# Performance work log

Measured on AMD Instinct MI355X. Metric: run time of the kernel, lower is better.

The kernel has to match this reference:

```python
import jax, jax.numpy as jnp
import numpy as np

N_NODES = 100000
LATENT_DIM = 8
SAMPLE_SIZE = 8192
N_EDGES = 1000000
EPS = 1e-6


def setup_inputs() -> dict:
    key = jax.random.key(0)
    k1, k2, k3, k4, k5 = jax.random.split(key, 5)
    latent_Z = jax.random.normal(k1, (N_NODES, LATENT_DIM), dtype=jnp.float32)
    alpha = jax.random.normal(k2, (1,), dtype=jnp.float32)
    sample_idx = jax.random.randint(k3, (SAMPLE_SIZE,), 0, N_NODES, dtype=jnp.int64)
    sparse_sample_i = jax.random.randint(k4, (N_EDGES,), 0, N_NODES, dtype=jnp.int64)
    sparse_sample_j = jax.random.randint(k5, (N_EDGES,), 0, N_NODES, dtype=jnp.int64)
    return {"latent_Z": latent_Z, "alpha": alpha, "sample_idx": sample_idx,
            "sparse_sample_i": sparse_sample_i, "sparse_sample_j": sparse_sample_j}


def reference(latent_Z, alpha, sample_idx, sparse_sample_i, sparse_sample_j):
    # --- dense non-edge term over the sampled subgraph ---
    Zs = latent_Z[sample_idx]                              # [S, D]
    diff = Zs[:, None, :] - Zs[None, :, :] + EPS           # [S, S, D]
    dist = jnp.sqrt(jnp.sum(diff * diff, axis=-1))         # [S, S]
    mat = jnp.exp(-dist)                                   # [S, S]
    # original uses exp(ones) vectors in the matmul-with-ones trick -> factor e^2
    ones_exp_sq = jnp.exp(jnp.float32(1.0)) ** 2
    offdiag_sum = jnp.sum(mat) - jnp.sum(jnp.diagonal(mat))
    z_pdist1 = jnp.exp(alpha[0]) * 0.5 * ones_exp_sq * offdiag_sum
    # --- sparse positive-edge term ---
    ed = latent_Z[sparse_sample_i] - latent_Z[sparse_sample_j] + EPS  # [E, D]
    edist = jnp.sqrt(jnp.sum(ed * ed, axis=-1))                        # [E]
    z_pdist2 = jnp.sum(-edist + alpha[0])
    return z_pdist2 - z_pdist1
```

## Files before the change

kernel.cpp:

```cpp
#include <hip/hip_runtime.h>
#include <hip/hip_bf16.h>
#include <math.h>

#define NNODES   100000
#define S        8192
#define D        8
#define EPSF     1e-6f
#define LOG2E    1.442695040888963f
#define EPS_S    (LOG2E * EPSF)
#define NT2      256

#define ZBS_OFF  0
#define U_OFF    131104
#define V_OFF    163872
#define ZB_OFF   196640
#define BK_OFF   1796736

#define NDBLK    2048
#define NWPP     64
#define ZROW     8192

typedef __attribute__((ext_vector_type(8)))  short short8_t;
typedef __attribute__((ext_vector_type(16))) float f32x16;

__device__ __forceinline__ void block_reduce_2(float a, float b, float* sma,
                                               float* smb, float& ra, float& rb) {
    #pragma unroll
    for (int off = 32; off > 0; off >>= 1) {
        a += __shfl_down(a, off, 64);
        b += __shfl_down(b, off, 64);
    }
    int lane = threadIdx.x & 63, wid = threadIdx.x >> 6;
    if (lane == 0) { sma[wid] = a; smb[wid] = b; }
    __syncthreads();
    if (threadIdx.x == 0) {
        ra = 0.f; rb = 0.f;
        for (int w = 0; w < 4; ++w) { ra += sma[w]; rb += smb[w]; }
    }
}

__global__ __launch_bounds__(256) void gather_kernel(const float* __restrict__ Z,
                                                     const int* __restrict__ idx,
                                                     ushort* __restrict__ zbs,
                                                     float* __restrict__ u,
                                                     float* __restrict__ v,
                                                     ushort* __restrict__ zb16,
                                                     char* __restrict__ buckets) {
    int gid = blockIdx.x * 256 + threadIdx.x;

    if (gid < 385) {
        *(double*)(buckets + (size_t)gid * 128) = 0.0;
    }
    if (blockIdx.x == 2 && threadIdx.x == 0) {
        short8_t zz = { 0,0,0,0,0,0,0,0 };
        *(short8_t*)(zbs + (size_t)ZROW * 8) = zz;
    }

    if (gid < S) {
        int n = idx[gid];
        const float4* zp = (const float4*)(Z + (size_t)n * D);
        float4 a = zp[0], b = zp[1];
        float z[8] = { a.x, a.y, a.z, a.w, b.x, b.y, b.z, b.w };
        float ss = 0.f;
        short8_t h;
        #pragma unroll
        for (int k = 0; k < 8; ++k) {
            float zs = LOG2E * z[k];
            __hip_bfloat16 hb = __float2bfloat16(zs);
            float hf = __bfloat162float(hb);
            ss = fmaf(hf, hf, ss);
            h[k] = (short)__builtin_bit_cast(unsigned short, hb);
        }
        *(short8_t*)(zbs + (size_t)gid * 8) = h;
        u[gid] = ss + 8.f * EPS_S * EPS_S;
        v[gid] = ss;
    }

    if (gid < NNODES) {
        const float4* zp = (const float4*)(Z + (size_t)gid * D);
        float4 a = zp[0], b = zp[1];
        float z[8] = { a.x, a.y, a.z, a.w, b.x, b.y, b.z, b.w };
        short8_t o;
        #pragma unroll
        for (int k = 0; k < 8; ++k) {
            __hip_bfloat16 bb = __float2bfloat16(z[k]);
            o[k] = (short)__builtin_bit_cast(unsigned short, bb);
        }
        *(short8_t*)(zb16 + (size_t)gid * 8) = o;
    }
}

#define UNPACK8(u4, f)                                        \
    f[0] = __uint_as_float(u4.x << 16);                       \
    f[1] = __uint_as_float(u4.x & 0xffff0000u);               \
    f[2] = __uint_as_float(u4.y << 16);                       \
    f[3] = __uint_as_float(u4.y & 0xffff0000u);               \
    f[4] = __uint_as_float(u4.z << 16);                       \
    f[5] = __uint_as_float(u4.z & 0xffff0000u);               \
    f[6] = __uint_as_float(u4.w << 16);                       \
    f[7] = __uint_as_float(u4.w & 0xffff0000u);

__device__ __forceinline__ void dense_sweep32(const ushort* __restrict__ zbs,
                                              const float* __restrict__ v,
                                              short8_t afrag, const float4* u4,
                                              int ti, int tj0, int cnt, int c31, int g,
                                              float& ax, float& ay, float& az, float& aw) {
    const ushort* bp = zbs + (size_t)(g ? ZROW : (tj0 * 32 + c31)) * 8;
    size_t step = g ? 0 : 256;
    const float* vp = v + tj0 * 32 + c31;
    short8_t bnext = *(const short8_t*)bp;
    float    vnext = vp[0];
    #pragma unroll 4
    for (int t = 0; t < cnt; ++t) {
        short8_t bc = bnext;
        float    vtc = vnext;
        if (t + 1 < cnt) {
            bnext = *(const short8_t*)(bp + (size_t)(t + 1) * step);
            vnext = vp[(t + 1) * 32];
        }
        float w = (tj0 + t == ti) ? 1.f : 2.f;
        f32x16 c = { 0.f, 0.f, 0.f, 0.f, 0.f, 0.f, 0.f, 0.f,
                     0.f, 0.f, 0.f, 0.f, 0.f, 0.f, 0.f, 0.f };
        c = __builtin_amdgcn_mfma_f32_32x32x16_bf16(afrag, bc, c, 0, 0, 0);
        #pragma unroll
        for (int q = 0; q < 4; ++q) {
            float s0 = u4[q].x + vtc, s1 = u4[q].y + vtc;
            float s2 = u4[q].z + vtc, s3 = u4[q].w + vtc;
            float d0 = fmaf(c[4*q+0], -2.f, s0);
            float d1 = fmaf(c[4*q+1], -2.f, s1);
            float d2 = fmaf(c[4*q+2], -2.f, s2);
            float d3 = fmaf(c[4*q+3], -2.f, s3);
            ax = fmaf(w, __builtin_amdgcn_exp2f(-__builtin_amdgcn_sqrtf(__builtin_fabsf(d0))), ax);
            ay = fmaf(w, __builtin_amdgcn_exp2f(-__builtin_amdgcn_sqrtf(__builtin_fabsf(d1))), ay);
            az = fmaf(w, __builtin_amdgcn_exp2f(-__builtin_amdgcn_sqrtf(__builtin_fabsf(d2))), az);
            aw = fmaf(w, __builtin_amdgcn_exp2f(-__builtin_amdgcn_sqrtf(__builtin_fabsf(d3))), aw);
        }
    }
}

__global__ __launch_bounds__(256) void fused_kernel(
        const ushort* __restrict__ zbs, const float* __restrict__ u,
        const float* __restrict__ v, const ushort* __restrict__ zb16,
        const int* __restrict__ ei, const int* __restrict__ ej, int ne,
        const float* __restrict__ alpha, char* __restrict__ buckets,
        float* __restrict__ out) {
    __shared__ float reda[4], redb[4];
    __shared__ unsigned composeFlag;
    int tid = threadIdx.x, bx = blockIdx.x;

    float sacc = 0.f;
    {
        const uint4* zb = (const uint4*)zb16;
        int nchunk = ne >> 2;
        int stride = NDBLK * 256;
        for (int c = bx * 256 + tid; c < nchunk; c += stride) {
            int4 ia = ((const int4*)ei)[c];
            int4 ib = ((const int4*)ej)[c];
            int aidx[4] = { ia.x, ia.y, ia.z, ia.w };
            int bidx[4] = { ib.x, ib.y, ib.z, ib.w };
            uint4 ua[4], ub[4];
            #pragma unroll
            for (int q = 0; q < 4; ++q) { ua[q] = zb[aidx[q]]; ub[q] = zb[bidx[q]]; }
            #pragma unroll
            for (int q = 0; q < 4; ++q) {
                float fa[8], fb[8];
                UNPACK8(ua[q], fa);
                UNPACK8(ub[q], fb);
                float s2 = 0.f;
                #pragma unroll
                for (int k = 0; k < 8; ++k) {
                    float d = fa[k] - fb[k] + EPSF;
                    s2 = fmaf(d, d, s2);
                }
                sacc += __builtin_amdgcn_sqrtf(s2);
            }
        }
        for (int e = (nchunk << 2) + bx * 256 + tid; e < ne; e += stride) {
            uint4 ua = zb[ei[e]];
            uint4 ub = zb[ej[e]];
            float fa[8], fb[8];
            UNPACK8(ua, fa);
            UNPACK8(ub, fb);
            float s2 = 0.f;
            #pragma unroll
            for (int k = 0; k < 8; ++k) {
                float d = fa[k] - fb[k] + EPSF;
                s2 = fmaf(d, d, s2);
            }
            sacc += __builtin_amdgcn_sqrtf(s2);
        }
    }

    int wave = tid >> 6, lane = tid & 63;
    int g = lane >> 5, c31 = lane & 31;

    int p  = bx >> 4;
    int wv = (bx & 15) * 4 + wave;
    int k0 = (wv * 257) / NWPP;
    int k1 = ((wv + 1) * 257) / NWPP;
    int n1 = NT2 - p;

    float ax = 0.f, ay = 0.f, az = 0.f, aw = 0.f;

    int eA = k1 < n1 ? k1 : n1;
    if (k0 < eA) {
        int ti = p;
        short8_t afrag = *(const short8_t*)(zbs + (size_t)(ti * 32 + c31) * 8);
        float4 u4[4];
        #pragma unroll
        for (int q = 0; q < 4; ++q) u4[q] = *(const float4*)(u + ti * 32 + 8 * q + 4 * g);
        dense_sweep32(zbs, v, afrag, u4, ti, p + k0, eA - k0, c31, g, ax, ay, az, aw);
    }
    int sB = k0 > n1 ? k0 : n1;
    if (sB < k1) {
        int ti = (NT2 - 1) - p;
        short8_t afrag = *(const short8_t*)(zbs + (size_t)(ti * 32 + c31) * 8);
        float4 u4[4];
        #pragma unroll
        for (int q = 0; q < 4; ++q) u4[q] = *(const float4*)(u + ti * 32 + 8 * q + 4 * g);
        dense_sweep32(zbs, v, afrag, u4, ti, ti + (sB - n1), k1 - sB, c31, g, ax, ay, az, aw);
    }

    float sd = 0.f, ss = 0.f;
    block_reduce_2((ax + ay) + (az + aw), sacc, reda, redb, sd, ss);

    double* dbuck = (double*)(buckets);
    double* sbuck = (double*)(buckets + 128 * 128);
    unsigned* gdone = (unsigned*)(buckets + 384 * 128);

    if (tid == 0) {
        int b = bx & 127;
        (void)atomicAdd((double*)((char*)dbuck + b * 128), (double)sd);
        (void)atomicAdd((double*)((char*)sbuck + b * 128), (double)ss);
        __builtin_amdgcn_s_waitcnt(0);
        unsigned oc = atomicAdd((unsigned*)(buckets + (256 + (bx >> 4)) * 128), 1u);
        unsigned gg = 0xFFFFu;
        if (oc == 15u) {
            __builtin_amdgcn_s_waitcnt(0);
            gg = atomicAdd(gdone, 1u);
        }
        composeFlag = (gg == 127u) ? 1u : 0u;
    }
    __syncthreads();

    if (composeFlag) {
        __shared__ double acc2[2];
        int w = tid >> 6;
        double val = 0.0;
        if (w == 0) {
            val  = atomicAdd((double*)((char*)dbuck + lane * 128), 0.0);
            val += atomicAdd((double*)((char*)dbuck + (lane + 64) * 128), 0.0);
        } else if (w == 1) {
            val  = atomicAdd((double*)((char*)sbuck + lane * 128), 0.0);
            val += atomicAdd((double*)((char*)sbuck + (lane + 64) * 128), 0.0);
        }
        #pragma unroll
        for (int off = 32; off > 0; off >>= 1) val += __shfl_down(val, off, 64);
        if (w == 0 && lane == 0) acc2[0] = val;
        if (w == 1 && lane == 0) acc2[1] = val;
        __syncthreads();
        if (tid == 0) {
            double Dsum = acc2[0], Ssum = acc2[1];
            double trace = (double)S * exp(-sqrt(8.0) * (double)EPSF);
            double offdiag = Dsum - trace;
            double a = (double)alpha[0];
            double z_pdist2 = (double)ne * a - Ssum;
            double z_pdist1 = exp(a) * 0.5 * 7.3890560989306495 * offdiag;
            out[0] = (float)(z_pdist2 - z_pdist1);
        }
    }
}

extern "C" void kernel_launch(void* const* d_in, const int* in_sizes, int n_in,
                              void* d_out, int out_size, void* d_ws, size_t ws_size,
                              hipStream_t stream) {
    const float* latent_Z = (const float*)d_in[0];
    const float* alpha    = (const float*)d_in[1];
    const int*   sidx     = (const int*)d_in[2];
    const int*   ei       = (const int*)d_in[3];
    const int*   ej       = (const int*)d_in[4];
    int ne = in_sizes[3];
    float* out = (float*)d_out;
    char*  ws  = (char*)d_ws;

    ushort* zbs   = (ushort*)(ws + ZBS_OFF);
    float*  u     = (float*)(ws + U_OFF);
    float*  v     = (float*)(ws + V_OFF);
    ushort* zb16  = (ushort*)(ws + ZB_OFF);
    char*   bk    = ws + BK_OFF;

    gather_kernel<<<(NNODES + 255) / 256, 256, 0, stream>>>(latent_Z, sidx,
                                                            zbs, u, v, zb16, bk);
    fused_kernel<<<NDBLK, 256, 0, stream>>>(zbs, u, v, zb16, ei, ej, ne,
                                            alpha, bk, out);
}
```

Measured before the change: 30.49 us.

## Reassign dense tile work to column-tile pairs with row sweeps

Restructures the dense upper-triangular tile sweep so each wave holds two fixed column tiles (B fragments and v) in registers and iterates over row tiles, loading the A fragment and u each step, instead of fixing a row tile and streaming column tiles. Block-to-work mapping changes to pair column tiles 2q and 254-2q with a 258-step balanced split over 128 waves per group. The zero-padded ZROW trick is dropped and launch bounds gain an occupancy hint of 6. This trades the B-prefetch pipelining for more reuse per MFMA pair and adds register pressure and occupancy constraints.

Result: no change. 30.39 us (-0.3%).

```diff
diff --git a/kernel.cpp b/kernel.cpp
--- a/kernel.cpp
+++ b/kernel.cpp
@@ -17,8 +17,7 @@
 #define BK_OFF   1796736
 
 #define NDBLK    2048
-#define NWPP     64
-#define ZROW     8192
+#define NL       258
 
 typedef __attribute__((ext_vector_type(8)))  short short8_t;
 typedef __attribute__((ext_vector_type(16))) float f32x16;
@@ -50,10 +49,6 @@
 
     if (gid < 385) {
         *(double*)(buckets + (size_t)gid * 128) = 0.0;
-    }
-    if (blockIdx.x == 2 && threadIdx.x == 0) {
-        short8_t zz = { 0,0,0,0,0,0,0,0 };
-        *(short8_t*)(zbs + (size_t)ZROW * 8) = zz;
     }
 
     if (gid < S) {
@@ -100,45 +95,53 @@
     f[6] = __uint_as_float(u4.w << 16);                       \
     f[7] = __uint_as_float(u4.w & 0xffff0000u);
 
-__device__ __forceinline__ void dense_sweep32(const ushort* __restrict__ zbs,
-                                              const float* __restrict__ v,
-                                              short8_t afrag, const float4* u4,
-                                              int ti, int tj0, int cnt, int c31, int g,
+__device__ __forceinline__ void accum32(short8_t af, short8_t bf, float vt,
+                                        const float4* u4, float wgt,
+                                        float& ax, float& ay, float& az, float& aw) {
+    f32x16 c = { 0.f, 0.f, 0.f, 0.f, 0.f, 0.f, 0.f, 0.f,
+                 0.f, 0.f, 0.f, 0.f, 0.f, 0.f, 0.f, 0.f };
+    c = __builtin_amdgcn_mfma_f32_32x32x16_bf16(af, bf, c, 0, 0, 0);
+    #pragma unroll
+    for (int q = 0; q < 4; ++q) {
+        float s0 = u4[q].x + vt, s1 = u4[q].y + vt;
+        float s2 = u4[q].z + vt, s3 = u4[q].w + vt;
+        float d0 = fmaf(c[4*q+0], -2.f, s0);
+        float d1 = fmaf(c[4*q+1], -2.f, s1);
+        float d2 = fmaf(c[4*q+2], -2.f, s2);
+        float d3 = fmaf(c[4*q+3], -2.f, s3);
+        ax = fmaf(wgt, __builtin_amdgcn_exp2f(-__builtin_amdgcn_sqrtf(__builtin_fabsf(d0))), ax);
+        ay = fmaf(wgt, __builtin_amdgcn_exp2f(-__builtin_amdgcn_sqrtf(__builtin_fabsf(d1))), ay);
+        az = fmaf(wgt, __builtin_amdgcn_exp2f(-__builtin_amdgcn_sqrtf(__builtin_fabsf(d2))), az);
+        aw = fmaf(wgt, __builtin_amdgcn_exp2f(-__builtin_amdgcn_sqrtf(__builtin_fabsf(d3))), aw);
+    }
+}
+
+__device__ __forceinline__ void dense_segment(const ushort* __restrict__ zbs,
+                                              const float* __restrict__ u,
+                                              const float* __restrict__ vv,
+                                              int k0, int k1, int tiOff, int jt0,
+                                              int c31, int g,
                                               float& ax, float& ay, float& az, float& aw) {
-    const ushort* bp = zbs + (size_t)(g ? ZROW : (tj0 * 32 + c31)) * 8;
-    size_t step = g ? 0 : 256;
-    const float* vp = v + tj0 * 32 + c31;
-    short8_t bnext = *(const short8_t*)bp;
-    float    vnext = vp[0];
-    #pragma unroll 4
-    for (int t = 0; t < cnt; ++t) {
-        short8_t bc = bnext;
-        float    vtc = vnext;
-        if (t + 1 < cnt) {
-            bnext = *(const short8_t*)(bp + (size_t)(t + 1) * step);
-            vnext = vp[(t + 1) * 32];
-        }
-        float w = (tj0 + t == ti) ? 1.f : 2.f;
-        f32x16 c = { 0.f, 0.f, 0.f, 0.f, 0.f, 0.f, 0.f, 0.f,
-                     0.f, 0.f, 0.f, 0.f, 0.f, 0.f, 0.f, 0.f };
-        c = __builtin_amdgcn_mfma_f32_32x32x16_bf16(afrag, bc, c, 0, 0, 0);
-        #pragma unroll
-        for (int q = 0; q < 4; ++q) {
-            float s0 = u4[q].x + vtc, s1 = u4[q].y + vtc;
-            float s2 = u4[q].z + vtc, s3 = u4[q].w + vtc;
-            float d0 = fmaf(c[4*q+0], -2.f, s0);
-            float d1 = fmaf(c[4*q+1], -2.f, s1);
-            float d2 = fmaf(c[4*q+2], -2.f, s2);
-            float d3 = fmaf(c[4*q+3], -2.f, s3);
-            ax = fmaf(w, __builtin_amdgcn_exp2f(-__builtin_amdgcn_sqrtf(__builtin_fabsf(d0))), ax);
-            ay = fmaf(w, __builtin_amdgcn_exp2f(-__builtin_amdgcn_sqrtf(__builtin_fabsf(d1))), ay);
-            az = fmaf(w, __builtin_amdgcn_exp2f(-__builtin_amdgcn_sqrtf(__builtin_fabsf(d2))), az);
-            aw = fmaf(w, __builtin_amdgcn_exp2f(-__builtin_amdgcn_sqrtf(__builtin_fabsf(d3))), aw);
-        }
-    }
-}
-
-__global__ __launch_bounds__(256) void fused_kernel(
+    short8_t zz = { 0,0,0,0,0,0,0,0 };
+    short8_t b0 = *(const short8_t*)(zbs + (size_t)(jt0 * 32 + c31) * 8);
+    short8_t b1 = *(const short8_t*)(zbs + (size_t)((jt0 + 1) * 32 + c31) * 8);
+    if (g) { b0 = zz; b1 = zz; }
+    float vt0 = vv[jt0 * 32 + c31];
+    float vt1 = vv[(jt0 + 1) * 32 + c31];
+    for (int k = k0; k < k1; ++k) {
+        int ti = k - tiOff;
+        short8_t af = *(const short8_t*)(zbs + (size_t)(ti * 32 + c31) * 8);
+        float4 u4[4];
+        #pragma unroll
+        for (int q = 0; q < 4; ++q) u4[q] = *(const float4*)(u + ti * 32 + 8 * q + 4 * g);
+        if (jt0 >= ti)
+            accum32(af, b0, vt0, u4, (jt0 == ti) ? 1.f : 2.f, ax, ay, az, aw);
+        if (jt0 + 1 >= ti)
+            accum32(af, b1, vt1, u4, (jt0 + 1 == ti) ? 1.f : 2.f, ax, ay, az, aw);
+    }
+}
+
+__global__ __launch_bounds__(256, 6) void fused_kernel(
         const ushort* __restrict__ zbs, const float* __restrict__ u,
         const float* __restrict__ v, const ushort* __restrict__ zb16,
         const int* __restrict__ ei, const int* __restrict__ ej, int ne,
@@ -194,32 +197,23 @@
     int wave = tid >> 6, lane = tid & 63;
     int g = lane >> 5, c31 = lane & 31;
 
-    int p  = bx >> 4;
-    int wv = (bx & 15) * 4 + wave;
-    int k0 = (wv * 257) / NWPP;
-    int k1 = ((wv + 1) * 257) / NWPP;
-    int n1 = NT2 - p;
+    int q  = bx >> 5;
+    int wv = (bx & 31) * 4 + wave;
+    int ja0 = 2 * q;
+    int jb0 = 254 - 2 * q;
+    int nA  = 2 * q + 2;
+
+    int k0 = (wv * NL) >> 7;
+    int k1 = ((wv + 1) * NL) >> 7;
 
     float ax = 0.f, ay = 0.f, az = 0.f, aw = 0.f;
 
-    int eA = k1 < n1 ? k1 : n1;
-    if (k0 < eA) {
-        int ti = p;
-        short8_t afrag = *(const short8_t*)(zbs + (size_t)(ti * 32 + c31) * 8);
-        float4 u4[4];
-        #pragma unroll
-        for (int q = 0; q < 4; ++q) u4[q] = *(const float4*)(u + ti * 32 + 8 * q + 4 * g);
-        dense_sweep32(zbs, v, afrag, u4, ti, p + k0, eA - k0, c31, g, ax, ay, az, aw);
-    }
-    int sB = k0 > n1 ? k0 : n1;
-    if (sB < k1) {
-        int ti = (NT2 - 1) - p;
-        short8_t afrag = *(const short8_t*)(zbs + (size_t)(ti * 32 + c31) * 8);
-        float4 u4[4];
-        #pragma unroll
-        for (int q = 0; q < 4; ++q) u4[q] = *(const float4*)(u + ti * 32 + 8 * q + 4 * g);
-        dense_sweep32(zbs, v, afrag, u4, ti, ti + (sB - n1), k1 - sB, c31, g, ax, ay, az, aw);
-    }
+    int eA = k1 < nA ? k1 : nA;
+    if (k0 < eA)
+        dense_segment(zbs, u, v, k0, eA, 0, ja0, c31, g, ax, ay, az, aw);
+    int sB = k0 > nA ? k0 : nA;
+    if (sB < k1)
+        dense_segment(zbs, u, v, sB, k1, nA, jb0, c31, g, ax, ay, az, aw);
 
     float sd = 0.f, ss = 0.f;
     block_reduce_2((ax + ay) + (az + aw), sacc, reda, redb, sd, ss);
```
